# Optimization experiments

Hardware: AMD Instinct MI355X
Metric: run time of the kernel (lower is better)

Reference implementation:

```python
import jax, jax.numpy as jnp
import numpy as np

B, T, D = 8, 2048, 1024

def _ln(x, g, b, eps=1e-5):
    mu = x.mean(-1, keepdims=True)
    var = ((x - mu) ** 2).mean(-1, keepdims=True)
    return (x - mu) * jax.lax.rsqrt(var + eps) * g + b

def setup_inputs() -> dict:
    key = jax.random.key(0)
    ks = jax.random.split(key, 8)
    s = 1.0 / np.sqrt(D)
    return {
        "x": jax.random.normal(ks[0], (B, T, D), jnp.float32),
        "Wq": jax.random.normal(ks[1], (D, D), jnp.float32) * s,
        "bq": jnp.zeros((D,), jnp.float32),
        "Wk": jax.random.normal(ks[2], (D, D), jnp.float32) * s,
        "bk": jnp.zeros((D,), jnp.float32),
        "Wv": jax.random.normal(ks[3], (D, D), jnp.float32) * s,
        "bv": jnp.zeros((D,), jnp.float32),
        "pos_bias": jax.random.normal(ks[4], (T, T), jnp.float32) * 0.1,
        "ln1_g": jnp.ones((D,), jnp.float32),
        "ln1_b": jnp.zeros((D,), jnp.float32),
        "W1": jax.random.normal(ks[5], (D, 4 * D), jnp.float32) * s,
        "b1": jnp.zeros((4 * D,), jnp.float32),
        "W2": jax.random.normal(ks[6], (4 * D, D), jnp.float32) * (1.0 / np.sqrt(4 * D)),
        "b2": jnp.zeros((D,), jnp.float32),
        "ln2_g": jnp.ones((D,), jnp.float32),
        "ln2_b": jnp.zeros((D,), jnp.float32),
    }

def reference(x, Wq, bq, Wk, bk, Wv, bv, pos_bias, ln1_g, ln1_b,
              W1, b1, W2, b2, ln2_g, ln2_b):
    # --- pre-norm AFT-full attention + residual ---
    h = _ln(x, ln1_g, ln1_b)
    q = h @ Wq + bq                      # [B,T,D]
    k = h @ Wk + bk
    v = h @ Wv + bv
    # global-max stabilization (cancels in the ratio)
    ek = jnp.exp(k - jax.lax.stop_gradient(k.max()))
    ew = jnp.exp(pos_bias - jax.lax.stop_gradient(pos_bias.max()))  # [T,T]
    num = jnp.einsum('ts,bsd->btd', ew, ek * v)
    den = jnp.einsum('ts,bsd->btd', ew, ek)
    attn = jax.nn.sigmoid(q) * (num / den)
    x = attn + x
    # --- pre-norm MLP + residual ---
    h = _ln(x, ln2_g, ln2_b)
    h = jax.nn.relu(h @ W1 + b1) @ W2 + b2
    return h + x
```

## Files before the change

kernel.cpp:

```cpp
#include <hip/hip_runtime.h>
#include <hip/hip_bf16.h>
#include <stdint.h>

typedef __hip_bfloat16 bf16;
typedef __attribute__((ext_vector_type(4))) float f32x4;
typedef __attribute__((ext_vector_type(8))) short bf16x8;

#define BB   8
#define TT   2048
#define DD   1024
#define MM   (BB * TT)

enum { EPI_Q = 0, EPI_K, EPI_V, EPI_ND, EPI_MLP1, EPI_MLP2 };

static __device__ __forceinline__ void async_ld16(const bf16* g, bf16* l) {
  __builtin_amdgcn_global_load_lds(
      (const __attribute__((address_space(1))) void*)g,
      (__attribute__((address_space(3))) void*)l, 16, 0, 0);
}

template<int EPI>
__global__ __launch_bounds__(256, 2)
void gemm_bt(const bf16* __restrict__ A, const bf16* __restrict__ B,
             int M, int N, int K,
             long long strideAz, long long strideBz,
             float* __restrict__ Cf,
             bf16* __restrict__ Cb, long long strideCz,
             const float* __restrict__ bias,
             const float* __restrict__ add,
             bf16* __restrict__ ekv)
{
  (void)M;
  __shared__ __align__(16) bf16 As[128 * 64];
  __shared__ __align__(16) bf16 Bs[128 * 64];

  const int tid  = threadIdx.x;
  const int wave = tid >> 6;
  const int lane = tid & 63;
  int bn, bm, bz;
  if constexpr (EPI == EPI_ND) {
    bz = blockIdx.x; bn = blockIdx.y; bm = blockIdx.z;
  } else {
    bn = blockIdx.x; bm = blockIdx.y; bz = 0;
  }
  A += (size_t)bz * strideAz;
  B += (size_t)bz * strideBz;

  const int wm = (wave >> 1) * 64;
  const int wn = (wave & 1) * 64;

  const int sr = lane >> 3;
  const int sc = (((lane & 7) ^ sr) & 7) * 8;
  const size_t a_row = (size_t)bm * 128 + wave * 32 + sr;
  const size_t b_row = (size_t)bn * 128 + wave * 32 + sr;
  const bf16* Ag = A + a_row * (size_t)K + sc;
  const bf16* Bg = B + b_row * (size_t)K + sc;
  bf16* Al = &As[(wave * 32) * 64];
  bf16* Bl = &Bs[(wave * 32) * 64];
  const size_t K8 = (size_t)8 * K;

  const int fm  = lane & 15;
  const int q4  = lane >> 4;
  const int fm7 = fm & 7;

  f32x4 acc[4][4];
#pragma unroll
  for (int i = 0; i < 4; ++i)
#pragma unroll
    for (int j = 0; j < 4; ++j) acc[i][j] = {0.f, 0.f, 0.f, 0.f};

  for (int k0 = 0; k0 < K; k0 += 64) {
#pragma unroll
    for (int o = 0; o < 4; ++o) {
      async_ld16(Ag + k0 + o * K8, Al + o * 8 * 64);
      async_ld16(Bg + k0 + o * K8, Bl + o * 8 * 64);
    }
    __builtin_amdgcn_s_waitcnt(0);
    __syncthreads();

#pragma unroll
    for (int h = 0; h < 2; ++h) {
      bf16x8 af[4], bfv[4];
#pragma unroll
      for (int i = 0; i < 4; ++i) {
        const int ca = ((h * 4 + q4) ^ fm7) * 8;
        af[i]  = *(const bf16x8*)&As[(wm + i * 16 + fm) * 64 + ca];
        bfv[i] = *(const bf16x8*)&Bs[(wn + i * 16 + fm) * 64 + ca];
      }
#pragma unroll
      for (int i = 0; i < 4; ++i)
#pragma unroll
        for (int j = 0; j < 4; ++j)
          acc[i][j] = __builtin_amdgcn_mfma_f32_16x16x32_bf16(
              af[i], bfv[j], acc[i][j], 0, 0, 0);
    }
    __syncthreads();
  }

  const int cr = (lane >> 4) * 4;
  const int cc = lane & 15;
#pragma unroll
  for (int i = 0; i < 4; ++i) {
#pragma unroll
    for (int j = 0; j < 4; ++j) {
#pragma unroll
      for (int r = 0; r < 4; ++r) {
        const int gm = bm * 128 + wm + i * 16 + cr + r;
        const int gn = bn * 128 + wn + j * 16 + cc;
        float v = acc[i][j][r];
        if constexpr (EPI == EPI_Q) {
          v += bias[gn];
          Cb[(size_t)gm * N + gn] = __float2bfloat16(v);
        } else if constexpr (EPI == EPI_K) {
          v = __expf(v + bias[gm]);
          const int b = gn >> 11, t = gn & (TT - 1);
          ekv[((size_t)b << 22) + (size_t)(1024 + gm) * TT + t] =
              __float2bfloat16(v);
        } else if constexpr (EPI == EPI_V) {
          v += bias[gm];
          const int b = gn >> 11, t = gn & (TT - 1);
          const size_t base = ((size_t)b << 22);
          const float ek =
              __bfloat162float(ekv[base + (size_t)(1024 + gm) * TT + t]);
          ekv[base + (size_t)gm * TT + t] = __float2bfloat16(v * ek);
        } else if constexpr (EPI == EPI_ND) {
          Cb[(size_t)bz * strideCz + (size_t)gm * N + gn] =
              __float2bfloat16(v);
        } else if constexpr (EPI == EPI_MLP1) {
          v = fmaxf(v + bias[gn], 0.0f);
          Cb[(size_t)gm * N + gn] = __float2bfloat16(v);
        } else {
          v += bias[gn] + add[(size_t)gm * N + gn];
          Cf[(size_t)gm * N + gn] = v;
        }
      }
    }
  }
}

__global__ __launch_bounds__(256)
void transpose_cast(const float* __restrict__ W, bf16* __restrict__ Wt,
                    int K, int N)
{
  __shared__ float tile[32][33];
  const int n0 = blockIdx.x * 32, k0 = blockIdx.y * 32;
  const int tx = threadIdx.x, ty = threadIdx.y;
#pragma unroll
  for (int i = 0; i < 32; i += 8)
    tile[ty + i][tx] = W[(size_t)(k0 + ty + i) * N + n0 + tx];
  __syncthreads();
#pragma unroll
  for (int i = 0; i < 32; i += 8)
    Wt[(size_t)(n0 + ty + i) * K + k0 + tx] =
        __float2bfloat16(tile[tx][ty + i]);
}

__global__ __launch_bounds__(256)
void ew_kernel(const float* __restrict__ pb, bf16* __restrict__ ew)
{
  const size_t gid = (size_t)blockIdx.x * 256 + threadIdx.x;
  const float4 v = *(const float4*)(pb + gid * 4);
  union { bf16 h[4]; unsigned long long u; } pk;
  pk.h[0] = __float2bfloat16(__expf(v.x));
  pk.h[1] = __float2bfloat16(__expf(v.y));
  pk.h[2] = __float2bfloat16(__expf(v.z));
  pk.h[3] = __float2bfloat16(__expf(v.w));
  *(unsigned long long*)(ew + gid * 4) = pk.u;
}

__global__ __launch_bounds__(256)
void ln_kernel(const float* __restrict__ x, const float* __restrict__ g,
               const float* __restrict__ b, bf16* __restrict__ out)
{
  const int row = blockIdx.x;
  const int tid = threadIdx.x;
  const float4 v = ((const float4*)(x + (size_t)row * DD))[tid];
  float s  = v.x + v.y + v.z + v.w;
  float s2 = v.x * v.x + v.y * v.y + v.z * v.z + v.w * v.w;
#pragma unroll
  for (int o = 32; o; o >>= 1) {
    s  += __shfl_down(s, o);
    s2 += __shfl_down(s2, o);
  }
  __shared__ float red[8];
  if ((tid & 63) == 0) { red[tid >> 6] = s; red[4 + (tid >> 6)] = s2; }
  __syncthreads();
  const float ts  = red[0] + red[1] + red[2] + red[3];
  const float ts2 = red[4] + red[5] + red[6] + red[7];
  const float mu = ts * (1.0f / DD);
  const float rs = rsqrtf(ts2 * (1.0f / DD) - mu * mu + 1e-5f);
  const float4 gv = ((const float4*)g)[tid];
  const float4 bv = ((const float4*)b)[tid];
  union { bf16 h[4]; unsigned long long u; } pk;
  pk.h[0] = __float2bfloat16((v.x - mu) * rs * gv.x + bv.x);
  pk.h[1] = __float2bfloat16((v.y - mu) * rs * gv.y + bv.y);
  pk.h[2] = __float2bfloat16((v.z - mu) * rs * gv.z + bv.z);
  pk.h[3] = __float2bfloat16((v.w - mu) * rs * gv.w + bv.w);
  ((unsigned long long*)(out + (size_t)row * DD))[tid] = pk.u;
}

__global__ __launch_bounds__(256)
void combine_ln_kernel(const bf16* __restrict__ q, const bf16* __restrict__ nd,
                       const float* __restrict__ x,
                       const float* __restrict__ g, const float* __restrict__ b,
                       float* __restrict__ x2, bf16* __restrict__ hout)
{
  const int row = blockIdx.x;
  const int tid = threadIdx.x;
  const int c = tid * 4;
  const bf16* ndr = nd + (size_t)row * 2048;
  union { unsigned long long u; bf16 h[4]; } un, ud, uq;
  un.u = *(const unsigned long long*)(ndr + c);
  ud.u = *(const unsigned long long*)(ndr + 1024 + c);
  uq.u = *(const unsigned long long*)(q + (size_t)row * DD + c);
  const float4 xv = *(const float4*)(x + (size_t)row * DD + c);
  float4 o;
  o.x = xv.x + (__bfloat162float(un.h[0]) / __bfloat162float(ud.h[0])) /
                   (1.0f + __expf(-__bfloat162float(uq.h[0])));
  o.y = xv.y + (__bfloat162float(un.h[1]) / __bfloat162float(ud.h[1])) /
                   (1.0f + __expf(-__bfloat162float(uq.h[1])));
  o.z = xv.z + (__bfloat162float(un.h[2]) / __bfloat162float(ud.h[2])) /
                   (1.0f + __expf(-__bfloat162float(uq.h[2])));
  o.w = xv.w + (__bfloat162float(un.h[3]) / __bfloat162float(ud.h[3])) /
                   (1.0f + __expf(-__bfloat162float(uq.h[3])));
  *(float4*)(x2 + (size_t)row * DD + c) = o;

  float s  = o.x + o.y + o.z + o.w;
  float s2 = o.x * o.x + o.y * o.y + o.z * o.z + o.w * o.w;
#pragma unroll
  for (int off = 32; off; off >>= 1) {
    s  += __shfl_down(s, off);
    s2 += __shfl_down(s2, off);
  }
  __shared__ float red[8];
  if ((tid & 63) == 0) { red[tid >> 6] = s; red[4 + (tid >> 6)] = s2; }
  __syncthreads();
  const float ts  = red[0] + red[1] + red[2] + red[3];
  const float ts2 = red[4] + red[5] + red[6] + red[7];
  const float mu = ts * (1.0f / DD);
  const float rs = rsqrtf(ts2 * (1.0f / DD) - mu * mu + 1e-5f);
  const float4 gv = ((const float4*)g)[tid];
  const float4 bv = ((const float4*)b)[tid];
  union { bf16 h[4]; unsigned long long u; } pk;
  pk.h[0] = __float2bfloat16((o.x - mu) * rs * gv.x + bv.x);
  pk.h[1] = __float2bfloat16((o.y - mu) * rs * gv.y + bv.y);
  pk.h[2] = __float2bfloat16((o.z - mu) * rs * gv.z + bv.z);
  pk.h[3] = __float2bfloat16((o.w - mu) * rs * gv.w + bv.w);
  ((unsigned long long*)(hout + (size_t)row * DD))[tid] = pk.u;
}

extern "C" void kernel_launch(void* const* d_in, const int* in_sizes, int n_in,
                              void* d_out, int out_size, void* d_ws,
                              size_t ws_size, hipStream_t stream)
{
  (void)in_sizes; (void)n_in; (void)out_size; (void)ws_size;
  const float* x   = (const float*)d_in[0];
  const float* Wq  = (const float*)d_in[1];
  const float* bq  = (const float*)d_in[2];
  const float* Wk  = (const float*)d_in[3];
  const float* bk  = (const float*)d_in[4];
  const float* Wv  = (const float*)d_in[5];
  const float* bv  = (const float*)d_in[6];
  const float* pb  = (const float*)d_in[7];
  const float* g1  = (const float*)d_in[8];
  const float* be1 = (const float*)d_in[9];
  const float* W1  = (const float*)d_in[10];
  const float* bm1 = (const float*)d_in[11];
  const float* W2  = (const float*)d_in[12];
  const float* bm2 = (const float*)d_in[13];
  const float* g2  = (const float*)d_in[14];
  const float* be2 = (const float*)d_in[15];
  float* out = (float*)d_out;

  const size_t MiB = 1024 * 1024;
  char* w = (char*)d_ws;
  bf16* hbf = (bf16*)w;  w += (size_t)MM * DD * 2;
  bf16* wqt = (bf16*)w;  w += (size_t)DD * DD * 2;
  bf16* wkt = (bf16*)w;  w += (size_t)DD * DD * 2;
  bf16* wvt = (bf16*)w;  w += (size_t)DD * DD * 2;
  bf16* w1t = (bf16*)w;  w += (size_t)4096 * DD * 2;
  bf16* w2t = (bf16*)w;  w += (size_t)DD * 4096 * 2;
  char* scr = w;
  bf16* qbf = (bf16*)scr;
  bf16* ewb = (bf16*)(scr + 32 * MiB);
  bf16* ekv = (bf16*)(scr + 40 * MiB);
  bf16* nd  = (bf16*)(scr + 104 * MiB);
  bf16* mid = (bf16*)scr;
  float* x2 = out;

  const dim3 tb(32, 8);
  transpose_cast<<<dim3(DD / 32, DD / 32), tb, 0, stream>>>(Wq, wqt, DD, DD);
  transpose_cast<<<dim3(DD / 32, DD / 32), tb, 0, stream>>>(Wk, wkt, DD, DD);
  transpose_cast<<<dim3(DD / 32, DD / 32), tb, 0, stream>>>(Wv, wvt, DD, DD);
  transpose_cast<<<dim3(4096 / 32, DD / 32), tb, 0, stream>>>(W1, w1t, DD, 4096);
  transpose_cast<<<dim3(DD / 32, 4096 / 32), tb, 0, stream>>>(W2, w2t, 4096, DD);

  ew_kernel<<<(TT * TT / 4) / 256, 256, 0, stream>>>(pb, ewb);
  ln_kernel<<<MM, 256, 0, stream>>>(x, g1, be1, hbf);

  gemm_bt<EPI_Q><<<dim3(DD / 128, MM / 128, 1), 256, 0, stream>>>(
      hbf, wqt, MM, DD, DD, 0, 0, nullptr, qbf, 0, bq, nullptr, nullptr);
  gemm_bt<EPI_K><<<dim3(MM / 128, DD / 128, 1), 256, 0, stream>>>(
      wkt, hbf, DD, MM, DD, 0, 0, nullptr, nullptr, 0, bk, nullptr, ekv);
  gemm_bt<EPI_V><<<dim3(MM / 128, DD / 128, 1), 256, 0, stream>>>(
      wvt, hbf, DD, MM, DD, 0, 0, nullptr, nullptr, 0, bv, nullptr, ekv);
  gemm_bt<EPI_ND><<<dim3(BB, TT / 128, TT / 128), 256, 0, stream>>>(
      ewb, ekv, TT, TT, TT, 0, (long long)TT * TT, nullptr, nd,
      (long long)TT * TT, nullptr, nullptr, nullptr);

  combine_ln_kernel<<<MM, 256, 0, stream>>>(qbf, nd, x, g2, be2, x2, hbf);

  gemm_bt<EPI_MLP1><<<dim3(4096 / 128, MM / 128, 1), 256, 0, stream>>>(
      hbf, w1t, MM, 4096, DD, 0, 0, nullptr, mid, 0, bm1, nullptr, nullptr);
  gemm_bt<EPI_MLP2><<<dim3(DD / 128, MM / 128, 1), 256, 0, stream>>>(
      mid, w2t, MM, DD, 4096, 0, 0, out, nullptr, 0, bm2, x2, nullptr);
}
```

Measured before the change: 791.3 us.

## Rewrite bf16 GEMM as 256x256 tile, 8-wave, 4-stage pipelined kernel with block swizzle

The shared GEMM moves from 128x128 tiles with 4 waves and a single synchronous LDS buffer to 256x256 tiles with 8 waves. A 4-deep ring of async global-to-LDS loads in 32-wide K slices is kept three stages ahead, with partial vmcnt waits and s_setprio around the MFMA bursts. A linear grid with an XCD-style block-index swizzle replaces the 3D grid. This aims to raise arithmetic intensity and hide load latency, at the cost of 128 KB of LDS per block, more accumulator registers, and fewer blocks in flight per CU.

```diff
diff --git a/kernel.cpp b/kernel.cpp
--- a/kernel.cpp
+++ b/kernel.cpp
@@ -20,7 +20,7 @@
 }
 
 template<int EPI>
-__global__ __launch_bounds__(256, 2)
+__global__ __launch_bounds__(512, 2)
 void gemm_bt(const bf16* __restrict__ A, const bf16* __restrict__ B,
              int M, int N, int K,
              long long strideAz, long long strideBz,
@@ -31,82 +31,120 @@
              bf16* __restrict__ ekv)
 {
   (void)M;
-  __shared__ __align__(16) bf16 As[128 * 64];
-  __shared__ __align__(16) bf16 Bs[128 * 64];
+  __shared__ __align__(16) bf16 lds[65536];
 
   const int tid  = threadIdx.x;
   const int wave = tid >> 6;
   const int lane = tid & 63;
+
+  const int nwg = (int)gridDim.x;
+  const int bid = (int)blockIdx.x;
+  const int swz = (bid & 7) * (nwg >> 3) + (bid >> 3);
   int bn, bm, bz;
   if constexpr (EPI == EPI_ND) {
-    bz = blockIdx.x; bn = blockIdx.y; bm = blockIdx.z;
+    bn = swz & 7; bm = (swz >> 3) & 7; bz = swz >> 6;
   } else {
-    bn = blockIdx.x; bm = blockIdx.y; bz = 0;
+    const int nbn = N >> 8;
+    const int lnb = 31 - __clz(nbn);
+    bn = swz & (nbn - 1); bm = swz >> lnb; bz = 0;
   }
   A += (size_t)bz * strideAz;
   B += (size_t)bz * strideBz;
 
-  const int wm = (wave >> 1) * 64;
-  const int wn = (wave & 1) * 64;
-
-  const int sr = lane >> 3;
-  const int sc = (((lane & 7) ^ sr) & 7) * 8;
-  const size_t a_row = (size_t)bm * 128 + wave * 32 + sr;
-  const size_t b_row = (size_t)bn * 128 + wave * 32 + sr;
-  const bf16* Ag = A + a_row * (size_t)K + sc;
-  const bf16* Bg = B + b_row * (size_t)K + sc;
-  bf16* Al = &As[(wave * 32) * 64];
-  bf16* Bl = &Bs[(wave * 32) * 64];
-  const size_t K8 = (size_t)8 * K;
-
-  const int fm  = lane & 15;
-  const int q4  = lane >> 4;
-  const int fm7 = fm & 7;
-
-  f32x4 acc[4][4];
-#pragma unroll
-  for (int i = 0; i < 4; ++i)
+  const int wm = (wave >> 2) * 128;
+  const int wn = (wave & 3) * 64;
+
+  const int lr = lane >> 2;
+  const int lc = (lane & 3) * 8;
+  const bf16* Ag0 = A + ((size_t)bm * 256 + wave * 32 + lr) * K + lc;
+  const bf16* Bg0 = B + ((size_t)bn * 256 + wave * 32 + lr) * K + lc;
+  const size_t K16 = (size_t)16 * K;
+  const int ldsAW = wave * 1024;
+  const int ldsBW = 32768 + wave * 1024;
+  const int NT = K >> 5;
+
+  auto stageA = [&](int tt) {
+    const int bo = (tt & 3) * 8192;
+    const bf16* g = Ag0 + (size_t)(tt & (NT - 1)) * 32;
+    async_ld16(g,       &lds[bo + ldsAW]);
+    async_ld16(g + K16, &lds[bo + ldsAW + 512]);
+  };
+  auto stageB = [&](int tt) {
+    const int bo = (tt & 3) * 8192;
+    const bf16* g = Bg0 + (size_t)(tt & (NT - 1)) * 32;
+    async_ld16(g,       &lds[bo + ldsBW]);
+    async_ld16(g + K16, &lds[bo + ldsBW + 512]);
+  };
+
+  f32x4 acc[8][4];
+#pragma unroll
+  for (int i = 0; i < 8; ++i)
 #pragma unroll
     for (int j = 0; j < 4; ++j) acc[i][j] = {0.f, 0.f, 0.f, 0.f};
 
-  for (int k0 = 0; k0 < K; k0 += 64) {
-#pragma unroll
-    for (int o = 0; o < 4; ++o) {
-      async_ld16(Ag + k0 + o * K8, Al + o * 8 * 64);
-      async_ld16(Bg + k0 + o * K8, Bl + o * 8 * 64);
-    }
-    __builtin_amdgcn_s_waitcnt(0);
-    __syncthreads();
-
-#pragma unroll
-    for (int h = 0; h < 2; ++h) {
-      bf16x8 af[4], bfv[4];
-#pragma unroll
-      for (int i = 0; i < 4; ++i) {
-        const int ca = ((h * 4 + q4) ^ fm7) * 8;
-        af[i]  = *(const bf16x8*)&As[(wm + i * 16 + fm) * 64 + ca];
-        bfv[i] = *(const bf16x8*)&Bs[(wn + i * 16 + fm) * 64 + ca];
-      }
-#pragma unroll
-      for (int i = 0; i < 4; ++i)
-#pragma unroll
-        for (int j = 0; j < 4; ++j)
-          acc[i][j] = __builtin_amdgcn_mfma_f32_16x16x32_bf16(
-              af[i], bfv[j], acc[i][j], 0, 0, 0);
-    }
-    __syncthreads();
+  stageA(0); stageB(0);
+  stageA(1); stageB(1);
+  stageA(2); stageB(2);
+  __builtin_amdgcn_sched_barrier(0);
+  asm volatile("s_waitcnt vmcnt(8)" ::: "memory");
+  __builtin_amdgcn_s_barrier();
+  __builtin_amdgcn_sched_barrier(0);
+
+  const int fm32 = (lane & 15) * 32;
+  const int q8   = (lane >> 4) * 8;
+
+  for (int t = 0; t < NT; ++t) {
+    const int ab = (t & 3) * 8192 + wm * 32 + fm32 + q8;
+    const int bb = 32768 + (t & 3) * 8192 + wn * 32 + fm32 + q8;
+    const int tw = t + 3;
+
+    bf16x8 bfr[4], af[4];
+#pragma unroll
+    for (int j = 0; j < 4; ++j) bfr[j] = *(const bf16x8*)&lds[bb + j * 512];
+#pragma unroll
+    for (int i = 0; i < 4; ++i) af[i] = *(const bf16x8*)&lds[ab + i * 512];
+    stageA(tw);
+    __builtin_amdgcn_sched_barrier(0);
+    asm volatile("s_waitcnt lgkmcnt(0)" ::: "memory");
+    __builtin_amdgcn_s_barrier();
+    __builtin_amdgcn_sched_barrier(0);
+    __builtin_amdgcn_s_setprio(1);
+#pragma unroll
+    for (int i = 0; i < 4; ++i)
+#pragma unroll
+      for (int j = 0; j < 4; ++j)
+        acc[i][j] = __builtin_amdgcn_mfma_f32_16x16x32_bf16(
+            af[i], bfr[j], acc[i][j], 0, 0, 0);
+    __builtin_amdgcn_s_setprio(0);
+
+#pragma unroll
+    for (int i = 0; i < 4; ++i)
+      af[i] = *(const bf16x8*)&lds[ab + 2048 + i * 512];
+    stageB(tw);
+    __builtin_amdgcn_sched_barrier(0);
+    asm volatile("s_waitcnt vmcnt(8) lgkmcnt(0)" ::: "memory");
+    __builtin_amdgcn_s_barrier();
+    __builtin_amdgcn_sched_barrier(0);
+    __builtin_amdgcn_s_setprio(1);
+#pragma unroll
+    for (int i = 0; i < 4; ++i)
+#pragma unroll
+      for (int j = 0; j < 4; ++j)
+        acc[4 + i][j] = __builtin_amdgcn_mfma_f32_16x16x32_bf16(
+            af[i], bfr[j], acc[4 + i][j], 0, 0, 0);
+    __builtin_amdgcn_s_setprio(0);
   }
 
   const int cr = (lane >> 4) * 4;
   const int cc = lane & 15;
 #pragma unroll
-  for (int i = 0; i < 4; ++i) {
+  for (int i = 0; i < 8; ++i) {
 #pragma unroll
     for (int j = 0; j < 4; ++j) {
 #pragma unroll
       for (int r = 0; r < 4; ++r) {
-        const int gm = bm * 128 + wm + i * 16 + cr + r;
-        const int gn = bn * 128 + wn + j * 16 + cc;
+        const int gm = bm * 256 + wm + i * 16 + cr + r;
+        const int gn = bn * 256 + wn + j * 16 + cc;
         float v = acc[i][j][r];
         if constexpr (EPI == EPI_Q) {
           v += bias[gn];
@@ -298,20 +336,20 @@
   ew_kernel<<<(TT * TT / 4) / 256, 256, 0, stream>>>(pb, ewb);
   ln_kernel<<<MM, 256, 0, stream>>>(x, g1, be1, hbf);
 
-  gemm_bt<EPI_Q><<<dim3(DD / 128, MM / 128, 1), 256, 0, stream>>>(
+  gemm_bt<EPI_Q><<<(MM / 256) * (DD / 256), 512, 0, stream>>>(
       hbf, wqt, MM, DD, DD, 0, 0, nullptr, qbf, 0, bq, nullptr, nullptr);
-  gemm_bt<EPI_K><<<dim3(MM / 128, DD / 128, 1), 256, 0, stream>>>(
+  gemm_bt<EPI_K><<<(DD / 256) * (MM / 256), 512, 0, stream>>>(
       wkt, hbf, DD, MM, DD, 0, 0, nullptr, nullptr, 0, bk, nullptr, ekv);
-  gemm_bt<EPI_V><<<dim3(MM / 128, DD / 128, 1), 256, 0, stream>>>(
+  gemm_bt<EPI_V><<<(DD / 256) * (MM / 256), 512, 0, stream>>>(
       wvt, hbf, DD, MM, DD, 0, 0, nullptr, nullptr, 0, bv, nullptr, ekv);
-  gemm_bt<EPI_ND><<<dim3(BB, TT / 128, TT / 128), 256, 0, stream>>>(
+  gemm_bt<EPI_ND><<<BB * (TT / 256) * (TT / 256), 512, 0, stream>>>(
       ewb, ekv, TT, TT, TT, 0, (long long)TT * TT, nullptr, nd,
       (long long)TT * TT, nullptr, nullptr, nullptr);
 
   combine_ln_kernel<<<MM, 256, 0, stream>>>(qbf, nd, x, g2, be2, x2, hbf);
 
-  gemm_bt<EPI_MLP1><<<dim3(4096 / 128, MM / 128, 1), 256, 0, stream>>>(
+  gemm_bt<EPI_MLP1><<<(MM / 256) * (4096 / 256), 512, 0, stream>>>(
       hbf, w1t, MM, 4096, DD, 0, 0, nullptr, mid, 0, bm1, nullptr, nullptr);
-  gemm_bt<EPI_MLP2><<<dim3(DD / 128, MM / 128, 1), 256, 0, stream>>>(
+  gemm_bt<EPI_MLP2><<<(MM / 256) * (DD / 256), 512, 0, stream>>>(
       mid, w2t, MM, DD, 4096, 0, 0, out, nullptr, 0, bm2, x2, nullptr);
 }
```

After: 761.0 us. -3.8%, faster.
